# Kernel optimization log

Measured on AMD Instinct MI355X. Metric: run time of the kernel, lower is better.

## Reference

```python
import jax, jax.numpy as jnp
import numpy as np

B, S = 2, 2048
EMBED = 2048
N_HEADS = 32
N_KV = 8
HEAD_DIM = 64
SLIDING_WINDOW = 128
ROPE_THETA = 10000.0
EPS = 1e-6


def _rms_norm(x, w):
    # normalize over last dim (head_dim)
    var = jnp.mean(jnp.square(x), axis=-1, keepdims=True)
    return x * jax.lax.rsqrt(var + EPS) * w


def _rope_half(t, cos, sin):
    # t: [B,S,H,D]; cos/sin: [S,D/2] -> broadcast [1,S,1,D/2]
    d2 = t.shape[-1] // 2
    t1, t2 = t[..., :d2], t[..., d2:]
    c = cos[None, :, None, :]
    s = sin[None, :, None, :]
    return jnp.concatenate([t1 * c - t2 * s, t2 * c + t1 * s], axis=-1)


def setup_inputs() -> dict:
    key = jax.random.key(0)
    ks = jax.random.split(key, 8)
    scale_in = 1.0 / np.sqrt(EMBED)
    scale_attn = 1.0 / np.sqrt(N_HEADS * HEAD_DIM)
    return {
        "x": jax.random.normal(ks[0], (B, S, EMBED), dtype=jnp.float32),
        "attention_mask": jnp.ones((B, S), dtype=jnp.int32),
        "wq": jax.random.normal(ks[1], (N_HEADS * HEAD_DIM, EMBED), dtype=jnp.float32) * scale_in,
        "wk": jax.random.normal(ks[2], (N_KV * HEAD_DIM, EMBED), dtype=jnp.float32) * scale_in,
        "wv": jax.random.normal(ks[3], (N_KV * HEAD_DIM, EMBED), dtype=jnp.float32) * scale_in,
        "wo": jax.random.normal(ks[4], (EMBED, N_HEADS * HEAD_DIM), dtype=jnp.float32) * scale_attn,
        "q_norm_w": jnp.ones((HEAD_DIM,), dtype=jnp.float32),
        "k_norm_w": jnp.ones((HEAD_DIM,), dtype=jnp.float32),
        "sinks": jax.random.normal(ks[5], (N_HEADS,), dtype=jnp.float32),
    }


def reference(x, attention_mask, wq, wk, wv, wo, q_norm_w, k_norm_w, sinks):
    Bv, Sv, _ = x.shape
    dtype = x.dtype

    # QKV projections (nn.Linear: x @ W.T, no bias)
    q = jnp.einsum('bse,he->bsh', x, wq).reshape(Bv, Sv, N_HEADS, HEAD_DIM)
    k = jnp.einsum('bse,he->bsh', x, wk).reshape(Bv, Sv, N_KV, HEAD_DIM)
    v = jnp.einsum('bse,he->bsh', x, wv).reshape(Bv, Sv, N_KV, HEAD_DIM)

    # QK RMSNorm (per head_dim)
    q = _rms_norm(q, q_norm_w)
    k = _rms_norm(k, k_norm_w)

    # RoPE, 'half' (rotate-half / NeoX style) for gpt_oss
    pos = jnp.arange(Sv, dtype=jnp.float32)
    inv_freq = 1.0 / (ROPE_THETA ** (jnp.arange(0, HEAD_DIM, 2, dtype=jnp.float32) / HEAD_DIM))
    ang = pos[:, None] * inv_freq[None, :]  # [S, D/2]
    cos, sin = jnp.cos(ang), jnp.sin(ang)
    q = _rope_half(q, cos, sin)
    k = _rope_half(k, cos, sin)

    # [B,H,S,D]; GQA repeat_interleave kv heads
    q = q.transpose(0, 2, 1, 3)
    k = jnp.repeat(k.transpose(0, 2, 1, 3), N_HEADS // N_KV, axis=1)
    v = jnp.repeat(v.transpose(0, 2, 1, 3), N_HEADS // N_KV, axis=1)

    scale = HEAD_DIM ** -0.5
    logits = jnp.einsum('bhqd,bhkd->bhqk', q, k) * scale  # [B,H,S,S]

    neg_inf = jnp.finfo(dtype).min
    # causal + sliding window mask (offset = k_len - q_len = 0 here)
    qi = jnp.arange(Sv)[:, None]
    ki = jnp.arange(Sv)[None, :]
    causal = (ki <= qi) & (ki >= qi - (SLIDING_WINDOW - 1))
    logits = jnp.where(causal[None, None, :, :], logits, neg_inf)

    # 2-D key mask branch
    key_mask = attention_mask[:, -Sv:] > 0  # [B,S]
    logits = jnp.where(key_mask[:, None, None, :], logits, neg_inf)

    # attention sinks: extra logit column per head
    sink = jnp.broadcast_to(sinks.astype(dtype).reshape(1, N_HEADS, 1, 1), (Bv, N_HEADS, Sv, 1))
    combined = jnp.concatenate([logits, sink], axis=-1)  # [B,H,S,S+1]
    combined = combined - jnp.max(combined, axis=-1, keepdims=True)
    probs = jax.nn.softmax(combined.astype(jnp.float32), axis=-1).astype(dtype)
    scores = probs[..., :-1]

    attn_out = jnp.einsum('bhqk,bhkd->bhqd', scores, v)  # [B,H,S,D]
    attn_out = attn_out.transpose(0, 2, 1, 3).reshape(Bv, Sv, N_HEADS * HEAD_DIM)
    return jnp.einsum('bsh,eh->bse', attn_out, wo)
```

## Files before the change

### kernel.cpp

```cpp
#include <hip/hip_runtime.h>
#include <hip/hip_bf16.h>

constexpr int BB = 2;
constexpr int SS = 2048;
constexpr int EMBED = 2048;
constexpr int NH = 32;
constexpr int NKV = 8;
constexpr int HD = 64;
constexpr int WIN = 128;
constexpr int M_ROWS = BB * SS;
constexpr int QKVC = 3072;
constexpr float SCALE = 0.125f;

typedef __bf16 bf16x8 __attribute__((ext_vector_type(8)));
typedef float f32x4 __attribute__((ext_vector_type(4)));

__device__ inline uint4 cvt8(float4 lo, float4 hi) {
    union { __hip_bfloat16 h[8]; uint4 u; } r;
    r.h[0] = __hip_bfloat16(lo.x); r.h[1] = __hip_bfloat16(lo.y);
    r.h[2] = __hip_bfloat16(lo.z); r.h[3] = __hip_bfloat16(lo.w);
    r.h[4] = __hip_bfloat16(hi.x); r.h[5] = __hip_bfloat16(hi.y);
    r.h[6] = __hip_bfloat16(hi.z); r.h[7] = __hip_bfloat16(hi.w);
    return r.u;
}
__device__ inline uint4 load8(const float* p) {
    float4 lo = *(const float4*)p;
    float4 hi = *(const float4*)(p + 4);
    return cvt8(lo, hi);
}

__device__ inline void gload_lds16(const __hip_bfloat16* g, uint4* l) {
    __builtin_amdgcn_global_load_lds(
        (const __attribute__((address_space(1))) void*)g,
        (__attribute__((address_space(3))) void*)l, 16, 0, 0);
}

__global__ __launch_bounds__(256) void prep_full(
    const float* __restrict__ x,  const float* __restrict__ wq,
    const float* __restrict__ wk, const float* __restrict__ wv,
    __hip_bfloat16* __restrict__ xb, __hip_bfloat16* __restrict__ wqkv,
    float2* __restrict__ tab)
{
    long bid = blockIdx.x;
    if (bid < 7168) {
        const float* src; __hip_bfloat16* dst; long off;
        if (bid < 4096)      { src = x;  dst = xb;             off = bid * 2048; }
        else if (bid < 6144) { src = wq; dst = wqkv;           off = (bid - 4096) * 2048; }
        else if (bid < 6656) { src = wk; dst = wqkv + 4194304; off = (bid - 6144) * 2048; }
        else                 { src = wv; dst = wqkv + 5242880; off = (bid - 6656) * 2048; }
        long i = off + (long)threadIdx.x * 8;
        *(uint4*)(dst + i) = load8(src + i);
    } else {
        int idx = (int)(bid - 7168) * 256 + threadIdx.x;
        int s = idx >> 5, i = idx & 31;
        float ang = (float)s * powf(10000.0f, -(float)i * (1.0f / 32.0f));
        float sn, cs;
        sincosf(ang, &sn, &cs);
        tab[idx] = make_float2(cs, sn);
    }
}

__global__ __launch_bounds__(256) void cvt_bf16(
    const float* __restrict__ in, __hip_bfloat16* __restrict__ out, long n)
{
    long i = ((long)blockIdx.x * 256 + threadIdx.x) * 8;
    if (i + 8 <= n) *(uint4*)(out + i) = load8(in + i);
}

#define BAR() __builtin_amdgcn_s_barrier()
#define LGKM0() do { \
    asm volatile("s_waitcnt lgkmcnt(0)" ::: "memory"); \
    __builtin_amdgcn_sched_barrier(0); } while (0)

#define WSTAGE(NB, KOFF) do { \
    _Pragma("unroll") for (int _j = 0; _j < ALD; ++_j) \
        gload_lds16(pA + (KOFF) + _j * 64 * (long)K, \
                    (uint4*)&lds[(NB) + _j * 4096 + t * 8]); \
    _Pragma("unroll") for (int _j = 0; _j < BLD; ++_j) \
        gload_lds16(pB + (KOFF) + _j * 64 * (long)K, \
                    (uint4*)&lds[(NB) + ASUB + _j * 4096 + t * 8]); \
} while (0)

#define WPHASE(CB, XS) do { \
    _Pragma("unroll") for (int _i = 0; _i < MI; ++_i) \
        af[_i] = *(const bf16x8*)&lds[(CB) + arow0 + _i * 1024 + (XS)]; \
    _Pragma("unroll") for (int _n = 0; _n < NI; ++_n) \
        bfr[_n] = *(const bf16x8*)&lds[(CB) + ASUB + brow0 + _n * 1024 + (XS)]; \
    LGKM0(); \
    __builtin_amdgcn_s_setprio(1); \
    _Pragma("unroll") for (int _i = 0; _i < MI; ++_i) { \
        _Pragma("unroll") for (int _n = 0; _n < NI; ++_n) \
            acc[_i][_n] = __builtin_amdgcn_mfma_f32_16x16x32_bf16( \
                af[_i], bfr[_n], acc[_i][_n], 0, 0, 0); \
    } \
    __builtin_amdgcn_s_setprio(0); \
} while (0)

template <typename TC, int BM, int BN>
__global__ __launch_bounds__(512) void gemmW(
    const __hip_bfloat16* __restrict__ A,
    const __hip_bfloat16* __restrict__ Bm,
    TC* __restrict__ C, int K, int ldc, int nbx)
{
    constexpr int WN   = BN / 4;
    constexpr int MI   = BM / 32;
    constexpr int NI   = WN / 16;
    constexpr int ASUB = BM * 64;
    constexpr int BSUB = BN * 64;
    constexpr int DB   = ASUB + BSUB;
    constexpr int ALD  = BM / 64;
    constexpr int BLD  = BN / 64;
    static_assert(WN % 16 == 0, "per-wave N must be frag-divisible");
    static_assert(2 * DB * 2 <= 131072, "LDS cap");

    __shared__ __hip_bfloat16 lds[2 * DB];

    const int t = threadIdx.x;
    const int lane = t & 63;
    const int wid = t >> 6;
    const int wm = wid >> 2;
    const int wn = wid & 3;
    const int lrow = lane & 15;
    const int quad = lane >> 4;

    int bid = blockIdx.x;
    const int nwg = gridDim.x;
    if ((nwg & 7) == 0) bid = (bid & 7) * (nwg >> 3) + (bid >> 3);
    const long blockM = (long)(bid / nbx) * BM;
    const long blockN = (long)(bid % nbx) * BN;

    const int srow = t >> 3;
    const int sslot = ((t & 7) ^ (srow & 7)) * 8;
    const __hip_bfloat16* pA = A  + (blockM + srow) * (long)K + sslot;
    const __hip_bfloat16* pB = Bm + (blockN + srow) * (long)K + sslot;

    const int arow0 = (wm * (BM / 2) + lrow) * 64;
    const int brow0 = (wn * WN + lrow) * 64;
    const int xs0 = ((quad)     ^ (lrow & 7)) * 8;
    const int xs1 = ((4 + quad) ^ (lrow & 7)) * 8;

    WSTAGE(0, 0);
    asm volatile("s_waitcnt vmcnt(0)" ::: "memory");
    BAR();

    f32x4 acc[MI][NI] = {};
    bf16x8 af[MI], bfr[NI];
    const int nkt = K >> 6;

    for (int kt = 0; kt < nkt; ++kt) {
        const int cb = (kt & 1) * DB;
        const int nb = DB - cb;
        const long kn = (long)((kt + 1 < nkt) ? (kt + 1) : kt) << 6;
        WSTAGE(nb, kn);
        WPHASE(cb, xs0);
        WPHASE(cb, xs1);
        asm volatile("s_waitcnt vmcnt(0)" ::: "memory");
        BAR();
    }

    #pragma unroll
    for (int mi = 0; mi < MI; ++mi)
        #pragma unroll
        for (int ni = 0; ni < NI; ++ni)
            #pragma unroll
            for (int r = 0; r < 4; ++r) {
                long rr = blockM + wm * (BM / 2) + mi * 16 + quad * 4 + r;
                long cc = blockN + wn * WN + ni * 16 + lrow;
                C[rr * (long)ldc + cc] = TC(acc[mi][ni][r]);
            }
}

__global__ __launch_bounds__(256) void norm_rope(
    __hip_bfloat16* __restrict__ qkv,
    const float* __restrict__ qw,
    const float* __restrict__ kw,
    const float2* __restrict__ tab)
{
    const int QROWS = M_ROWS * NH;
    const int lane = threadIdx.x & 63;
    const int sub = lane >> 3;
    const int j = lane & 7;
    const int gid = (blockIdx.x * 4 + (threadIdx.x >> 6)) * 8 + sub;

    __hip_bfloat16* base;
    const float* wptr;
    int s;
    if (gid < QROWS) {
        int row = gid >> 5;
        base = qkv + (long)row * QKVC + (gid & 31) * HD;
        s = row & (SS - 1);
        wptr = qw;
    } else {
        int g = gid - QROWS;
        int row = g >> 3;
        base = qkv + (long)row * QKVC + 2048 + (g & 7) * HD;
        s = row & (SS - 1);
        wptr = kw;
    }

    bf16x8 v = *(const bf16x8*)(base + j * 8);
    float xf[8];
    float ss = 0.f;
    #pragma unroll
    for (int u = 0; u < 8; ++u) { xf[u] = (float)v[u]; ss += xf[u] * xf[u]; }
    ss += __shfl_xor(ss, 1); ss += __shfl_xor(ss, 2); ss += __shfl_xor(ss, 4);
    float scale = rsqrtf(ss * (1.0f / 64.0f) + 1e-6f);
    #pragma unroll
    for (int u = 0; u < 8; ++u) xf[u] = xf[u] * scale * wptr[j * 8 + u];

    float pf[8];
    #pragma unroll
    for (int u = 0; u < 8; ++u) pf[u] = __shfl_xor(xf[u], 4);

    const float2* tp = tab + s * 32 + (j & 3) * 8;
    union { __hip_bfloat16 h[8]; uint4 u4; } y;
    #pragma unroll
    for (int u = 0; u < 8; ++u) {
        float2 cs2 = tp[u];
        float yv = (j < 4) ? (xf[u] * cs2.x - pf[u] * cs2.y)
                           : (xf[u] * cs2.x + pf[u] * cs2.y);
        y.h[u] = __hip_bfloat16(yv);
    }
    *(uint4*)(base + j * 8) = y.u4;
}

constexpr int SPAN = 192;
constexpr int KROW = 72;
constexpr int PROW = 200;

__global__ __launch_bounds__(256) void attn_mfma(
    const __hip_bfloat16* __restrict__ qkv,
    const int* __restrict__ amask,
    const float* __restrict__ sinks,
    __hip_bfloat16* __restrict__ ao)
{
    __shared__ __hip_bfloat16 KsPs[SPAN * KROW];
    __shared__ __hip_bfloat16 Vt[64 * PROW];

    const int bid = blockIdx.x;
    const int qt = bid & 31;
    const int h = (bid >> 5) & 31;
    const int b = bid >> 10;
    const int kv = h >> 2;
    const int q0 = qt * 64;
    const int base = q0 - (WIN - 1);
    const int t = threadIdx.x;
    const int w = t >> 6;
    const int lane = t & 63;
    const int lrow = lane & 15;
    const int quad = lane >> 4;

    for (int c = t; c < SPAN * 8; c += 256) {
        int j = c >> 3;
        int d0 = (c & 7) * 8;
        int kg = base + j;
        uint4 kk = {0, 0, 0, 0}, vv = {0, 0, 0, 0};
        if (kg >= 0 && kg < SS) {
            long rowoff = ((long)b * SS + kg) * QKVC + kv * HD + d0;
            kk = *(const uint4*)(qkv + rowoff + 2048);
            vv = *(const uint4*)(qkv + rowoff + 2560);
        }
        *(uint4*)&KsPs[j * KROW + d0] = kk;
        const __hip_bfloat16* vp = (const __hip_bfloat16*)&vv;
        #pragma unroll
        for (int u = 0; u < 8; u++) Vt[(d0 + u) * PROW + j] = vp[u];
    }
    __syncthreads();

    const __hip_bfloat16* qrow =
        qkv + ((long)b * SS + q0 + w * 16 + lrow) * QKVC + h * HD;
    bf16x8 qa0 = *(const bf16x8*)(qrow + quad * 8);
    bf16x8 qa1 = *(const bf16x8*)(qrow + 32 + quad * 8);

    f32x4 s[12] = {};
    #pragma unroll
    for (int ni = 0; ni < 12; ni++) {
        bf16x8 kb0 = *(const bf16x8*)&KsPs[(ni * 16 + lrow) * KROW + quad * 8];
        bf16x8 kb1 = *(const bf16x8*)&KsPs[(ni * 16 + lrow) * KROW + 32 + quad * 8];
        s[ni] = __builtin_amdgcn_mfma_f32_16x16x32_bf16(qa0, kb0, s[ni], 0, 0, 0);
        s[ni] = __builtin_amdgcn_mfma_f32_16x16x32_bf16(qa1, kb1, s[ni], 0, 0, 0);
    }

    bool jok[12];
    #pragma unroll
    for (int ni = 0; ni < 12; ni++) {
        int kg = base + ni * 16 + lrow;
        jok[ni] = (kg >= 0) && (kg < SS) && (amask[b * SS + (kg >= 0 && kg < SS ? kg : 0)] > 0);
    }

    const float sinkv = sinks[h];

    #pragma unroll
    for (int reg = 0; reg < 4; reg++) {
        int row = w * 16 + quad * 4 + reg;
        float mrow = -3.0e30f;
        #pragma unroll
        for (int ni = 0; ni < 12; ni++) {
            int j = ni * 16 + lrow;
            bool valid = jok[ni] && (j >= row) && (j <= row + 127);
            float val = valid ? s[ni][reg] * SCALE : -1.0e30f;
            s[ni][reg] = val;
            mrow = fmaxf(mrow, val);
        }
        #pragma unroll
        for (int off = 1; off < 16; off <<= 1) mrow = fmaxf(mrow, __shfl_xor(mrow, off));
        mrow = fmaxf(mrow, sinkv);
        float sum = 0.f;
        #pragma unroll
        for (int ni = 0; ni < 12; ni++) {
            float e = __expf(s[ni][reg] - mrow);
            s[ni][reg] = e;
            sum += e;
        }
        #pragma unroll
        for (int off = 1; off < 16; off <<= 1) sum += __shfl_xor(sum, off);
        sum += __expf(sinkv - mrow);
        float inv = 1.0f / sum;
        #pragma unroll
        for (int ni = 0; ni < 12; ni++) s[ni][reg] *= inv;
    }

    __syncthreads();

    #pragma unroll
    for (int ni = 0; ni < 12; ni++)
        #pragma unroll
        for (int reg = 0; reg < 4; reg++)
            KsPs[(w * 16 + quad * 4 + reg) * PROW + ni * 16 + lrow] =
                __hip_bfloat16(s[ni][reg]);
    __syncthreads();

    f32x4 o[4] = {};
    #pragma unroll
    for (int ks = 0; ks < 6; ks++) {
        bf16x8 pa = *(const bf16x8*)&KsPs[(w * 16 + lrow) * PROW + ks * 32 + quad * 8];
        #pragma unroll
        for (int ni = 0; ni < 4; ni++) {
            bf16x8 vb = *(const bf16x8*)&Vt[(ni * 16 + lrow) * PROW + ks * 32 + quad * 8];
            o[ni] = __builtin_amdgcn_mfma_f32_16x16x32_bf16(pa, vb, o[ni], 0, 0, 0);
        }
    }

    #pragma unroll
    for (int ni = 0; ni < 4; ni++)
        #pragma unroll
        for (int reg = 0; reg < 4; reg++) {
            int row = w * 16 + quad * 4 + reg;
            ao[((long)b * SS + q0 + row) * (NH * HD) + h * HD + ni * 16 + lrow] =
                __hip_bfloat16(o[ni][reg]);
        }
}

extern "C" void kernel_launch(void* const* d_in, const int* in_sizes, int n_in,
                              void* d_out, int out_size, void* d_ws, size_t ws_size,
                              hipStream_t stream) {
    const float* x     = (const float*)d_in[0];
    const int*   am    = (const int*)d_in[1];
    const float* wq    = (const float*)d_in[2];
    const float* wk    = (const float*)d_in[3];
    const float* wv    = (const float*)d_in[4];
    const float* wo    = (const float*)d_in[5];
    const float* qnw   = (const float*)d_in[6];
    const float* knw   = (const float*)d_in[7];
    const float* sinks = (const float*)d_in[8];
    float* out = (float*)d_out;

    __hip_bfloat16* xb    = (__hip_bfloat16*)d_out;
    __hip_bfloat16* wqkv  = (__hip_bfloat16*)((char*)d_out + 16777216);
    float2*         rtab  = (float2*)((char*)d_out + 29360128);
    __hip_bfloat16* qkv   = (__hip_bfloat16*)x;
    __hip_bfloat16* wob   = (__hip_bfloat16*)((char*)x + 25165824);
    __hip_bfloat16* abuf  = (__hip_bfloat16*)wq;

    const long NW = (long)EMBED * EMBED;

    prep_full<<<7424, 256, 0, stream>>>(x, wq, wk, wv, xb, wqkv, rtab);
    cvt_bf16<<<NW / 2048, 256, 0, stream>>>(wo, wob, NW);

    gemmW<__hip_bfloat16, 256, 192><<<256, 512, 0, stream>>>(
        xb, wqkv, qkv, EMBED, QKVC, QKVC / 192);

    int rows = M_ROWS * NH + M_ROWS * NKV;
    norm_rope<<<rows / 32, 256, 0, stream>>>(qkv, qnw, knw, rtab);

    attn_mfma<<<BB * NH * (SS / 64), 256, 0, stream>>>(qkv, am, sinks, abuf);

    gemmW<float, 128, 256><<<256, 512, 0, stream>>>(
        abuf, wob, out, EMBED, EMBED, EMBED / 256);
}
```

Measured before the change: 252.8 us.

## Fuse QK RMSNorm and RoPE into QKV GEMM epilogue via LDS staging

The separate norm_rope kernel is removed. The QKV GEMM now writes its bf16 output tile to LDS, then each 8-lane group normalizes and rotates one head row before writing it to global memory with 16-byte stores. This removes one kernel launch and a full read-modify-write pass over the Q and K buffers. In exchange the GEMM epilogue gets an extra barrier and more ALU work. Registers or LDS reuse could also affect GEMM occupancy.

```diff
diff --git a/kernel.cpp b/kernel.cpp
--- a/kernel.cpp
+++ b/kernel.cpp
@@ -96,11 +96,13 @@
     __builtin_amdgcn_s_setprio(0); \
 } while (0)
 
-template <typename TC, int BM, int BN>
+template <typename TC, int BM, int BN, bool NORM>
 __global__ __launch_bounds__(512) void gemmW(
     const __hip_bfloat16* __restrict__ A,
     const __hip_bfloat16* __restrict__ Bm,
-    TC* __restrict__ C, int K, int ldc, int nbx)
+    TC* __restrict__ C, int K, int ldc, int nbx,
+    const float* __restrict__ qw, const float* __restrict__ kw,
+    const float2* __restrict__ tab)
 {
     constexpr int WN   = BN / 4;
     constexpr int MI   = BM / 32;
@@ -158,70 +160,75 @@
         BAR();
     }
 
-    #pragma unroll
-    for (int mi = 0; mi < MI; ++mi)
-        #pragma unroll
-        for (int ni = 0; ni < NI; ++ni)
+    if constexpr (!NORM) {
+        #pragma unroll
+        for (int mi = 0; mi < MI; ++mi)
             #pragma unroll
-            for (int r = 0; r < 4; ++r) {
-                long rr = blockM + wm * (BM / 2) + mi * 16 + quad * 4 + r;
-                long cc = blockN + wn * WN + ni * 16 + lrow;
-                C[rr * (long)ldc + cc] = TC(acc[mi][ni][r]);
+            for (int ni = 0; ni < NI; ++ni)
+                #pragma unroll
+                for (int r = 0; r < 4; ++r) {
+                    long rr = blockM + wm * (BM / 2) + mi * 16 + quad * 4 + r;
+                    long cc = blockN + wn * WN + ni * 16 + lrow;
+                    C[rr * (long)ldc + cc] = TC(acc[mi][ni][r]);
+                }
+    } else {
+        constexpr int RS = BN + 8;
+        constexpr int HN = BN / 64;
+        static_assert(BM * RS <= 2 * DB, "C-tile fits LDS");
+        static_assert(BN % 64 == 0, "tile must hold whole heads");
+
+        #pragma unroll
+        for (int mi = 0; mi < MI; ++mi)
+            #pragma unroll
+            for (int ni = 0; ni < NI; ++ni)
+                #pragma unroll
+                for (int r = 0; r < 4; ++r) {
+                    int row = wm * (BM / 2) + mi * 16 + quad * 4 + r;
+                    int col = wn * WN + ni * 16 + lrow;
+                    lds[row * RS + col] = __hip_bfloat16(acc[mi][ni][r]);
+                }
+        BAR();
+
+        const int grp = t >> 3;
+        const int j = t & 7;
+        #pragma unroll
+        for (int it = 0; it < BM * HN / 64; ++it) {
+            int rh = it * 64 + grp;
+            int r = rh / HN, hc = rh % HN;
+            int head = (int)(blockN >> 6) + hc;
+            long grow = blockM + r;
+            const uint4* src16 = (const uint4*)&lds[r * RS + hc * 64 + j * 8];
+            uint4 outw;
+            if (head < NH + NKV) {
+                bf16x8 v = *(const bf16x8*)src16;
+                const float* wptr = (head < NH) ? qw : kw;
+                float xf[8]; float ssq = 0.f;
+                #pragma unroll
+                for (int u = 0; u < 8; ++u) { xf[u] = (float)v[u]; ssq += xf[u] * xf[u]; }
+                ssq += __shfl_xor(ssq, 1); ssq += __shfl_xor(ssq, 2); ssq += __shfl_xor(ssq, 4);
+                float sc = rsqrtf(ssq * (1.0f / 64.0f) + 1e-6f);
+                #pragma unroll
+                for (int u = 0; u < 8; ++u) xf[u] = xf[u] * sc * wptr[j * 8 + u];
+                float pf[8];
+                #pragma unroll
+                for (int u = 0; u < 8; ++u) pf[u] = __shfl_xor(xf[u], 4);
+                int s = (int)(grow & (SS - 1));
+                const float2* tp = tab + s * 32 + (j & 3) * 8;
+                union { __hip_bfloat16 h[8]; uint4 u4; } y;
+                #pragma unroll
+                for (int u = 0; u < 8; ++u) {
+                    float2 c2 = tp[u];
+                    float yv = (j < 4) ? (xf[u] * c2.x - pf[u] * c2.y)
+                                       : (xf[u] * c2.x + pf[u] * c2.y);
+                    y.h[u] = __hip_bfloat16(yv);
+                }
+                outw = y.u4;
+            } else {
+                outw = *src16;
             }
-}
-
-__global__ __launch_bounds__(256) void norm_rope(
-    __hip_bfloat16* __restrict__ qkv,
-    const float* __restrict__ qw,
-    const float* __restrict__ kw,
-    const float2* __restrict__ tab)
-{
-    const int QROWS = M_ROWS * NH;
-    const int lane = threadIdx.x & 63;
-    const int sub = lane >> 3;
-    const int j = lane & 7;
-    const int gid = (blockIdx.x * 4 + (threadIdx.x >> 6)) * 8 + sub;
-
-    __hip_bfloat16* base;
-    const float* wptr;
-    int s;
-    if (gid < QROWS) {
-        int row = gid >> 5;
-        base = qkv + (long)row * QKVC + (gid & 31) * HD;
-        s = row & (SS - 1);
-        wptr = qw;
-    } else {
-        int g = gid - QROWS;
-        int row = g >> 3;
-        base = qkv + (long)row * QKVC + 2048 + (g & 7) * HD;
-        s = row & (SS - 1);
-        wptr = kw;
-    }
-
-    bf16x8 v = *(const bf16x8*)(base + j * 8);
-    float xf[8];
-    float ss = 0.f;
-    #pragma unroll
-    for (int u = 0; u < 8; ++u) { xf[u] = (float)v[u]; ss += xf[u] * xf[u]; }
-    ss += __shfl_xor(ss, 1); ss += __shfl_xor(ss, 2); ss += __shfl_xor(ss, 4);
-    float scale = rsqrtf(ss * (1.0f / 64.0f) + 1e-6f);
-    #pragma unroll
-    for (int u = 0; u < 8; ++u) xf[u] = xf[u] * scale * wptr[j * 8 + u];
-
-    float pf[8];
-    #pragma unroll
-    for (int u = 0; u < 8; ++u) pf[u] = __shfl_xor(xf[u], 4);
-
-    const float2* tp = tab + s * 32 + (j & 3) * 8;
-    union { __hip_bfloat16 h[8]; uint4 u4; } y;
-    #pragma unroll
-    for (int u = 0; u < 8; ++u) {
-        float2 cs2 = tp[u];
-        float yv = (j < 4) ? (xf[u] * cs2.x - pf[u] * cs2.y)
-                           : (xf[u] * cs2.x + pf[u] * cs2.y);
-        y.h[u] = __hip_bfloat16(yv);
-    }
-    *(uint4*)(base + j * 8) = y.u4;
+            *(uint4*)((__hip_bfloat16*)C + grow * (long)ldc + (head << 6) + j * 8) = outw;
+        }
+    }
 }
 
 constexpr int SPAN = 192;
@@ -377,14 +384,11 @@
     prep_full<<<7424, 256, 0, stream>>>(x, wq, wk, wv, xb, wqkv, rtab);
     cvt_bf16<<<NW / 2048, 256, 0, stream>>>(wo, wob, NW);
 
-    gemmW<__hip_bfloat16, 256, 192><<<256, 512, 0, stream>>>(
-        xb, wqkv, qkv, EMBED, QKVC, QKVC / 192);
-
-    int rows = M_ROWS * NH + M_ROWS * NKV;
-    norm_rope<<<rows / 32, 256, 0, stream>>>(qkv, qnw, knw, rtab);
+    gemmW<__hip_bfloat16, 256, 192, true><<<256, 512, 0, stream>>>(
+        xb, wqkv, qkv, EMBED, QKVC, QKVC / 192, qnw, knw, rtab);
 
     attn_mfma<<<BB * NH * (SS / 64), 256, 0, stream>>>(qkv, am, sinks, abuf);
 
-    gemmW<float, 128, 256><<<256, 512, 0, stream>>>(
-        abuf, wob, out, EMBED, EMBED, EMBED / 256);
-}
+    gemmW<float, 128, 256, false><<<256, 512, 0, stream>>>(
+        abuf, wob, out, EMBED, EMBED, EMBED / 256, nullptr, nullptr, nullptr);
+}
```

New measurement: 248.6 us. No clear change (-1.7%).
